# Performance work log

Measured on AMD Instinct MI355X. Metric: run time of the kernel, lower is better.

Reference implementation:

```python
import jax, jax.numpy as jnp
import numpy as np

INPUT_DIM, HIDDEN_DIM, OUTPUT_DIM = 64, 256, 32
BATCH, SEQ = 256, 1024
# AutoNCP(256, 32, sparsity_level=0.5): motor=32, command=max(int(0.4*224),1)=89, inter=135
LAYER_HID = [135, 89, 32]
LAYER_IN = [INPUT_DIM, 135, 89]


def setup_inputs() -> dict:
    key = jax.random.key(0)
    ks = iter(jax.random.split(key, 64))
    d = {}
    d["x"] = jax.random.normal(next(ks), (BATCH, SEQ, INPUT_DIM), dtype=jnp.float32)
    for l, (fin, hid) in enumerate(zip(LAYER_IN, LAYER_HID)):
        sp = jax.random.bernoulli(next(ks), 0.5, (hid, fin))
        d[f"mask{l}"] = jnp.concatenate([sp, jnp.ones((hid, hid), dtype=bool)], axis=1)
        scale = 1.0 / np.sqrt(fin + hid)
        for name in ("W1", "W2", "Wa", "Wb"):
            d[f"{name}_{l}"] = jax.random.normal(next(ks), (hid, fin + hid), dtype=jnp.float32) * scale
        for name in ("b1", "b2", "ba", "bb"):
            d[f"{name}_{l}"] = jnp.zeros((hid,), dtype=jnp.float32)
    d["fc_W"] = jax.random.normal(next(ks), (HIDDEN_DIM, HIDDEN_DIM), dtype=jnp.float32) * (1.0 / np.sqrt(HIDDEN_DIM))
    d["fc_b"] = jnp.zeros((HIDDEN_DIM,), dtype=jnp.float32)
    return d


def _cfc_cell(inp, h, mask, W1, b1, W2, b2, Wa, ba, Wb, bb):
    # ncps CfCCell, mode='default', no backbone, ts = 1.0
    x = jnp.concatenate([inp, h], axis=1)
    m = mask.astype(W1.dtype)
    ff1 = jnp.tanh(x @ (W1 * m).T + b1)
    ff2 = jnp.tanh(x @ (W2 * m).T + b2)
    t = jax.nn.sigmoid(x @ Wa.T + ba + x @ Wb.T + bb)  # sigmoid(t_a*ts + t_b), ts=1
    return ff1 * (1.0 - t) + t * ff2


def _forward(x, masks, layer_params, fc_W, fc_b):
    B = x.shape[0]
    init = tuple(jnp.zeros((B, h), dtype=x.dtype) for h in LAYER_HID)

    def step(carry, xt):
        hs = list(carry)
        inp = xt
        for l in range(3):  # inter -> command -> motor (WiredCfCCell)
            hs[l] = _cfc_cell(inp, hs[l], masks[l], *layer_params[l])
            inp = hs[l]
        return tuple(hs), None

    carry, _ = jax.lax.scan(step, init, jnp.swapaxes(x, 0, 1))  # scan over time [T,B,D]
    hn = jnp.concatenate(carry, axis=1)  # [B, HIDDEN_DIM] full state
    return hn @ fc_W.T + fc_b


def reference(x, mask0, mask1, mask2,
              W1_0, b1_0, W2_0, b2_0, Wa_0, ba_0, Wb_0, bb_0,
              W1_1, b1_1, W2_1, b2_1, Wa_1, ba_1, Wb_1, bb_1,
              W1_2, b1_2, W2_2, b2_2, Wa_2, ba_2, Wb_2, bb_2,
              fc_W, fc_b):
    masks = (mask0, mask1, mask2)
    lp = ((W1_0, b1_0, W2_0, b2_0, Wa_0, ba_0, Wb_0, bb_0),
          (W1_1, b1_1, W2_1, b2_1, Wa_1, ba_1, Wb_1, bb_1),
          (W1_2, b1_2, W2_2, b2_2, Wa_2, ba_2, Wb_2, bb_2))
    return _forward(x, masks, lp, fc_W, fc_b)
```

## Files before the change

kernel.cpp:

```cpp
#include <hip/hip_runtime.h>


typedef _Float16 half2v __attribute__((ext_vector_type(2)));
typedef _Float16 half8v __attribute__((ext_vector_type(8)));

#define NBLK   256
#define NTHR   1024
#define TSTEPS 1024
#define KPAD   224
#define KQUAR  56
#define NKB    7

struct Ptrs {
    const float* x;
    const unsigned int* msk[3];
    const float* W1[3];
    const float* W2[3];
    const float* Wa[3];
    const float* Wb[3];
    const float* b1[3];
    const float* b2[3];
    const float* ba[3];
    const float* bb[3];
    const float* fcW;
    const float* fcb;
};

__device__ __forceinline__ float fexp2(float x) {
#if __has_builtin(__builtin_amdgcn_exp2f)
    return __builtin_amdgcn_exp2f(x);
#else
    return exp2f(x);
#endif
}
__device__ __forceinline__ float frcp(float x) {
#if __has_builtin(__builtin_amdgcn_rcpf)
    return __builtin_amdgcn_rcpf(x);
#else
    return 1.0f / x;
#endif
}
__device__ __forceinline__ float fsig(float x) {
    return frcp(1.0f + fexp2(-1.442695041f * x));
}
__device__ __forceinline__ float ftanh(float x) {
    return 2.0f * frcp(1.0f + fexp2(-2.885390082f * x)) - 1.0f;
}

#if __has_builtin(__builtin_amdgcn_fdot2)
#define FD(a, b, c) __builtin_amdgcn_fdot2((a), (b), (c), false)
#else
__device__ __forceinline__ float fd_fallback(half2v a, half2v b, float c) {
    return c + (float)a[0] * (float)b[0] + (float)a[1] * (float)b[1];
}
#define FD(a, b, c) fd_fallback((a), (b), (c))
#endif

__device__ __forceinline__ half2v h2(_Float16 a, _Float16 b) { return half2v{a, b}; }

__device__ __forceinline__ half2v fold2(const float* Wp, const unsigned int* mkp,
                                        int nK, int K, int k0) {
    float u0 = 0.f, u1 = 0.f;
    if (k0 < K) {
        const int i0 = nK + k0;
        u0 = Wp[i0] * ((mkp[i0] != 0u) ? 1.0f : 0.0f);
    }
    if (k0 + 1 < K) {
        const int i1 = nK + k0 + 1;
        u1 = Wp[i1] * ((mkp[i1] != 0u) ? 1.0f : 0.0f);
    }
    return h2((_Float16)u0, (_Float16)u1);
}

#define DECL_KB(kb) \
    const half2v w1_##kb##_0 = fold2(W1p, mkp, nK, K, koff + kb * 8 + 0); \
    const half2v w1_##kb##_1 = fold2(W1p, mkp, nK, K, koff + kb * 8 + 2); \
    const half2v w1_##kb##_2 = fold2(W1p, mkp, nK, K, koff + kb * 8 + 4); \
    const half2v w1_##kb##_3 = fold2(W1p, mkp, nK, K, koff + kb * 8 + 6); \
    const half2v w2_##kb##_0 = fold2(W2p, mkp, nK, K, koff + kb * 8 + 0); \
    const half2v w2_##kb##_1 = fold2(W2p, mkp, nK, K, koff + kb * 8 + 2); \
    const half2v w2_##kb##_2 = fold2(W2p, mkp, nK, K, koff + kb * 8 + 4); \
    const half2v w2_##kb##_3 = fold2(W2p, mkp, nK, K, koff + kb * 8 + 6);

#define DOT_KB(kb) { \
    const half8v xv = *(const half8v*)(srcp + kb * 8); \
    const half8v wv = *(const half8v*)(wap + kb * 8); \
    ac00 = FD(h2(xv[0], xv[1]), w1_##kb##_0, ac00); \
    ac10 = FD(h2(xv[0], xv[1]), w2_##kb##_0, ac10); \
    ac20 = FD(h2(xv[0], xv[1]), h2(wv[0], wv[1]), ac20); \
    ac01 = FD(h2(xv[2], xv[3]), w1_##kb##_1, ac01); \
    ac11 = FD(h2(xv[2], xv[3]), w2_##kb##_1, ac11); \
    ac21 = FD(h2(xv[2], xv[3]), h2(wv[2], wv[3]), ac21); \
    ac00 = FD(h2(xv[4], xv[5]), w1_##kb##_2, ac00); \
    ac10 = FD(h2(xv[4], xv[5]), w2_##kb##_2, ac10); \
    ac20 = FD(h2(xv[4], xv[5]), h2(wv[4], wv[5]), ac20); \
    ac01 = FD(h2(xv[6], xv[7]), w1_##kb##_3, ac01); \
    ac11 = FD(h2(xv[6], xv[7]), w2_##kb##_3, ac11); \
    ac21 = FD(h2(xv[6], xv[7]), h2(wv[6], wv[7]), ac21); \
}

__global__ __launch_bounds__(NTHR)
__attribute__((amdgpu_waves_per_eu(4, 4), amdgpu_num_vgpr(96)))
void cfc_kernel(Ptrs P, float* __restrict__ out) {
    __shared__ __align__(16) _Float16 xc[2][3][KPAD];
    __shared__ __align__(16) _Float16 waL[256][KPAD];
    __shared__ __align__(16) float hn[256];

    const int tid  = threadIdx.x;
    const int b    = blockIdx.x;
    const int unit = tid >> 2;
    const int q    = tid & 3;

    int L, n;
    if (unit < 135)      { L = 0; n = unit; }
    else if (unit < 224) { L = 1; n = unit - 135; }
    else                 { L = 2; n = unit - 224; }
    const int K    = (L == 0) ? 199 : ((L == 1) ? 224 : 121);
    const int HOFF = (L == 0) ? 0   : ((L == 1) ? 135 : 224);

    {
        int* z = (int*)&xc[0][0][0];
        for (int i = tid; i < 2 * 3 * KPAD / 2; i += NTHR) z[i] = 0;
    }

    const int xlane = tid - (NTHR - 64);
    float xpend = 0.0f;

    const float* W1p        = P.W1[L];
    const float* W2p        = P.W2[L];
    const float* Wap        = P.Wa[L];
    const float* Wbp        = P.Wb[L];
    const unsigned int* mkp = P.msk[L];
    const int nK   = n * K;
    const int koff = q * KQUAR;

    DECL_KB(0) DECL_KB(1) DECL_KB(2) DECL_KB(3) DECL_KB(4) DECL_KB(5) DECL_KB(6)

#pragma unroll
    for (int i = 0; i < KQUAR / 2; ++i) {
        const int k0 = koff + 2 * i;
        float a0 = 0.f, a1 = 0.f;
        if (k0 < K)     a0 = Wap[nK + k0] + Wbp[nK + k0];
        if (k0 + 1 < K) a1 = Wap[nK + k0 + 1] + Wbp[nK + k0 + 1];
        *(half2v*)&waL[unit][k0] = h2((_Float16)a0, (_Float16)a1);
    }

    const float bv1 = P.b1[L][n];
    const float bv2 = P.b2[L][n];
    const float bva = P.ba[L][n] + P.bb[L][n];

    if (xlane >= 0) {
        xc[0][0][xlane] = (_Float16)P.x[((size_t)b * TSTEPS + 0) * 64 + xlane];
        xpend           = P.x[((size_t)b * TSTEPS + 1) * 64 + xlane];
    }
    __syncthreads();

    const _Float16* wap = &waL[unit][koff];
    const _Float16* s0p = &xc[0][L][koff];
    const _Float16* s1p = &xc[1][L][koff];

    for (int tick = 0; tick < TSTEPS + 2; ++tick) {
        if (xlane >= 0) {
            if (tick + 1 < TSTEPS)
                xc[(tick + 1) & 1][0][xlane] = (_Float16)xpend;
            if (tick + 2 < TSTEPS)
                xpend = P.x[((size_t)b * TSTEPS + (tick + 2)) * 64 + xlane];
        }

        const int s = tick - L;
        if (s >= 0 && s < TSTEPS) {
            const _Float16* srcp = (s & 1) ? s1p : s0p;
            float ac00 = 0.f, ac01 = 0.f, ac10 = 0.f, ac11 = 0.f, ac20 = 0.f, ac21 = 0.f;
            DOT_KB(0) DOT_KB(1) DOT_KB(2) DOT_KB(3) DOT_KB(4) DOT_KB(5) DOT_KB(6)

            float s1 = ac00 + ac01;
            float s2 = ac10 + ac11;
            float sa = ac20 + ac21;
            s1 += __shfl_xor(s1, 1, 64);
            s2 += __shfl_xor(s2, 1, 64);
            sa += __shfl_xor(sa, 1, 64);
            s1 += __shfl_xor(s1, 2, 64);
            s2 += __shfl_xor(s2, 2, 64);
            sa += __shfl_xor(sa, 2, 64);
            const float f1 = ftanh(s1 + bv1);
            const float f2 = ftanh(s2 + bv2);
            const float tg = fsig(sa + bva);
            const float h  = f1 + tg * (f2 - f1);
            const _Float16 hv = (_Float16)h;

            const int pA = s & 1;
            const int pB = (s + 1) & 1;
            if (q == 0) {
                if (L == 0)      xc[pA][1][n] = hv;
                else if (L == 1) xc[pA][2][n] = hv;
                if (s == TSTEPS - 1) hn[HOFF + n] = h;
            } else if (q == 1) {
                if (L == 0)      xc[pB][0][64 + n]  = hv;
                else if (L == 1) xc[pB][1][135 + n] = hv;
                else             xc[pB][2][89 + n]  = hv;
            }
        }
        __syncthreads();
    }

    {
        const int o = unit;
        const float4* wr = (const float4*)(P.fcW + (size_t)o * 256 + q * 64);
        const float4* hr = (const float4*)(hn + q * 64);
        float acc = (q == 0) ? P.fcb[o] : 0.0f;
#pragma unroll
        for (int d = 0; d < 16; ++d) {
            const float4 a = hr[d];
            const float4 w = wr[d];
            acc += a.x * w.x + a.y * w.y + a.z * w.z + a.w * w.w;
        }
        acc += __shfl_xor(acc, 1, 64);
        acc += __shfl_xor(acc, 2, 64);
        if (q == 0) out[(size_t)b * 256 + o] = acc;
    }
}

extern "C" void kernel_launch(void* const* d_in, const int* in_sizes, int n_in,
                              void* d_out, int out_size, void* d_ws, size_t ws_size,
                              hipStream_t stream) {
    (void)in_sizes; (void)n_in; (void)out_size; (void)d_ws; (void)ws_size;
    Ptrs P;
    P.x = (const float*)d_in[0];
    for (int l = 0; l < 3; ++l) {
        const int base = 1 + l * 9;
        P.msk[l] = (const unsigned int*)d_in[base + 0];
        P.W1[l]  = (const float*)d_in[base + 1];
        P.W2[l]  = (const float*)d_in[base + 2];
        P.Wa[l]  = (const float*)d_in[base + 3];
        P.Wb[l]  = (const float*)d_in[base + 4];
        P.b1[l]  = (const float*)d_in[base + 5];
        P.b2[l]  = (const float*)d_in[base + 6];
        P.ba[l]  = (const float*)d_in[base + 7];
        P.bb[l]  = (const float*)d_in[base + 8];
    }
    P.fcW = (const float*)d_in[28];
    P.fcb = (const float*)d_in[29];

    hipLaunchKernelGGL(cfc_kernel, dim3(NBLK), dim3(NTHR), 0, stream,
                       P, (float*)d_out);
}
```

Baseline: 1.797 ms.

## Split each neuron across two threads instead of four and pad weight rows

The block shrinks from 1024 to 512 threads. Each recurrent unit is now handled by 2 threads, each covering 112 of the K inputs, instead of 4 threads covering 56 each. This doubles the register-resident folded W1/W2 weights per thread and removes one cross-lane shuffle stage from the per-step reductions and the final FC. The LDS row stride for the combined Wa+Wb weights is padded from 224 to 232 halves, likely to reduce bank conflicts. In exchange, each step's serial dot chain per thread is longer and there are fewer waves to hide LDS latency, while the per-step barrier covers fewer waves.

```diff
diff --git a/kernel.cpp b/kernel.cpp
--- a/kernel.cpp
+++ b/kernel.cpp
@@ -5,11 +5,12 @@
 typedef _Float16 half8v __attribute__((ext_vector_type(8)));
 
 #define NBLK   256
-#define NTHR   1024
+#define NTHR   512
 #define TSTEPS 1024
 #define KPAD   224
-#define KQUAR  56
-#define NKB    7
+#define WSTRIDE 232
+#define KHALF  112
+#define NKB    14
 
 struct Ptrs {
     const float* x;
@@ -99,17 +100,16 @@
     ac21 = FD(h2(xv[6], xv[7]), h2(wv[6], wv[7]), ac21); \
 }
 
-__global__ __launch_bounds__(NTHR)
-__attribute__((amdgpu_waves_per_eu(4, 4), amdgpu_num_vgpr(96)))
+__global__ __launch_bounds__(NTHR, 2)
 void cfc_kernel(Ptrs P, float* __restrict__ out) {
     __shared__ __align__(16) _Float16 xc[2][3][KPAD];
-    __shared__ __align__(16) _Float16 waL[256][KPAD];
+    __shared__ __align__(16) _Float16 waL[256][WSTRIDE];
     __shared__ __align__(16) float hn[256];
 
     const int tid  = threadIdx.x;
     const int b    = blockIdx.x;
-    const int unit = tid >> 2;
-    const int q    = tid & 3;
+    const int unit = tid >> 1;
+    const int half = tid & 1;
 
     int L, n;
     if (unit < 135)      { L = 0; n = unit; }
@@ -123,21 +123,20 @@
         for (int i = tid; i < 2 * 3 * KPAD / 2; i += NTHR) z[i] = 0;
     }
 
-    const int xlane = tid - (NTHR - 64);
-    float xpend = 0.0f;
-
     const float* W1p        = P.W1[L];
     const float* W2p        = P.W2[L];
     const float* Wap        = P.Wa[L];
     const float* Wbp        = P.Wb[L];
     const unsigned int* mkp = P.msk[L];
     const int nK   = n * K;
-    const int koff = q * KQUAR;
-
-    DECL_KB(0) DECL_KB(1) DECL_KB(2) DECL_KB(3) DECL_KB(4) DECL_KB(5) DECL_KB(6)
+    const int koff = half * KHALF;
+
+    DECL_KB(0)  DECL_KB(1)  DECL_KB(2)  DECL_KB(3)  DECL_KB(4)
+    DECL_KB(5)  DECL_KB(6)  DECL_KB(7)  DECL_KB(8)  DECL_KB(9)
+    DECL_KB(10) DECL_KB(11) DECL_KB(12) DECL_KB(13)
 
 #pragma unroll
-    for (int i = 0; i < KQUAR / 2; ++i) {
+    for (int i = 0; i < KHALF / 2; ++i) {
         const int k0 = koff + 2 * i;
         float a0 = 0.f, a1 = 0.f;
         if (k0 < K)     a0 = Wap[nK + k0] + Wbp[nK + k0];
@@ -149,6 +148,8 @@
     const float bv2 = P.b2[L][n];
     const float bva = P.ba[L][n] + P.bb[L][n];
 
+    const int xlane = tid - (NTHR - 64);
+    float xpend = 0.0f;
     if (xlane >= 0) {
         xc[0][0][xlane] = (_Float16)P.x[((size_t)b * TSTEPS + 0) * 64 + xlane];
         xpend           = P.x[((size_t)b * TSTEPS + 1) * 64 + xlane];
@@ -171,7 +172,9 @@
         if (s >= 0 && s < TSTEPS) {
             const _Float16* srcp = (s & 1) ? s1p : s0p;
             float ac00 = 0.f, ac01 = 0.f, ac10 = 0.f, ac11 = 0.f, ac20 = 0.f, ac21 = 0.f;
-            DOT_KB(0) DOT_KB(1) DOT_KB(2) DOT_KB(3) DOT_KB(4) DOT_KB(5) DOT_KB(6)
+            DOT_KB(0)  DOT_KB(1)  DOT_KB(2)  DOT_KB(3)  DOT_KB(4)
+            DOT_KB(5)  DOT_KB(6)  DOT_KB(7)  DOT_KB(8)  DOT_KB(9)
+            DOT_KB(10) DOT_KB(11) DOT_KB(12) DOT_KB(13)
 
             float s1 = ac00 + ac01;
             float s2 = ac10 + ac11;
@@ -179,9 +182,6 @@
             s1 += __shfl_xor(s1, 1, 64);
             s2 += __shfl_xor(s2, 1, 64);
             sa += __shfl_xor(sa, 1, 64);
-            s1 += __shfl_xor(s1, 2, 64);
-            s2 += __shfl_xor(s2, 2, 64);
-            sa += __shfl_xor(sa, 2, 64);
             const float f1 = ftanh(s1 + bv1);
             const float f2 = ftanh(s2 + bv2);
             const float tg = fsig(sa + bva);
@@ -190,11 +190,11 @@
 
             const int pA = s & 1;
             const int pB = (s + 1) & 1;
-            if (q == 0) {
+            if (half == 0) {
                 if (L == 0)      xc[pA][1][n] = hv;
                 else if (L == 1) xc[pA][2][n] = hv;
                 if (s == TSTEPS - 1) hn[HOFF + n] = h;
-            } else if (q == 1) {
+            } else {
                 if (L == 0)      xc[pB][0][64 + n]  = hv;
                 else if (L == 1) xc[pB][1][135 + n] = hv;
                 else             xc[pB][2][89 + n]  = hv;
@@ -205,18 +205,17 @@
 
     {
         const int o = unit;
-        const float4* wr = (const float4*)(P.fcW + (size_t)o * 256 + q * 64);
-        const float4* hr = (const float4*)(hn + q * 64);
-        float acc = (q == 0) ? P.fcb[o] : 0.0f;
-#pragma unroll
-        for (int d = 0; d < 16; ++d) {
+        const float4* wr = (const float4*)(P.fcW + (size_t)o * 256 + half * 128);
+        const float4* hr = (const float4*)(hn + half * 128);
+        float acc = half ? 0.0f : P.fcb[o];
+#pragma unroll 8
+        for (int d = 0; d < 32; ++d) {
             const float4 a = hr[d];
             const float4 w = wr[d];
             acc += a.x * w.x + a.y * w.y + a.z * w.z + a.w * w.w;
         }
         acc += __shfl_xor(acc, 1, 64);
-        acc += __shfl_xor(acc, 2, 64);
-        if (q == 0) out[(size_t)b * 256 + o] = acc;
+        if (half == 0) out[(size_t)b * 256 + o] = acc;
     }
 }
 
```

Measured after the change: 1.649 ms. 1.09x faster.
